# Performance work log

Hardware: AMD Instinct MI355X
Metric: run time of the kernel (lower is better)

The kernel has to match this reference:

```python
import jax, jax.numpy as jnp
import numpy as np

D_K = 128  # query/key dim, used for the 1/sqrt(d_k) scale


def setup_inputs() -> dict:
    key = jax.random.key(0)
    k1, k2, k3, k4 = jax.random.split(key, 4)
    B, L, d_model, d_k, d_v = 4, 2048, 1024, 128, 128

    def xavier(k, shape):
        # matches nn.init.xavier_uniform_ for 2D weights
        limit = np.sqrt(6.0 / (shape[0] + shape[1]))
        return jax.random.uniform(k, shape, jnp.float32, -limit, limit)

    return {
        "X": jax.random.normal(k1, (B, L, d_model), jnp.float32),
        "W_Q": xavier(k2, (d_model, d_k)),
        "W_K": xavier(k3, (d_model, d_k)),
        "W_V": xavier(k4, (d_model, d_v)),
    }


def reference(X, W_Q, W_K, W_V):
    # X: (B, L, d_model)
    L = X.shape[1]
    Q = jnp.einsum("bld,dk->blk", X, W_Q)          # (B, L, d_k)
    K = jnp.einsum("bld,dk->blk", X, W_K)          # (B, L, d_k)
    V = jnp.einsum("bld,dv->blv", X, W_V)          # (B, L, d_v)
    scale = D_K ** -0.5
    scores = jnp.einsum("bqk,bpk->bqp", Q, K) * scale  # (B, L, L)
    # causal mask: positions above the diagonal set to -inf
    causal = jnp.tril(jnp.ones((L, L), dtype=bool))
    scores = jnp.where(causal, scores, -jnp.inf)
    A = jax.nn.softmax(scores, axis=-1)            # (B, L, L)
    Z = jnp.einsum("bqp,bpv->bqv", A, V)           # (B, L, d_v)
    return Z
```

## Files before the change

### kernel.cpp

```cpp
#include <hip/hip_runtime.h>
#include <hip/hip_bf16.h>

typedef __bf16 bf16;
typedef __attribute__((ext_vector_type(4))) __bf16 bf16x4;
typedef __attribute__((ext_vector_type(8))) __bf16 bf16x8;
typedef __attribute__((ext_vector_type(4))) float f32x4;

#define D_MODEL 1024
#define DK 128
#define LSEQ 2048
#define NQT 128
#define NB 4
#define SCALE2 (0.08838834764831845f * 1.4426950408889634f)

__global__ __launch_bounds__(256) void xb_kernel(
    const float* __restrict__ X, bf16* __restrict__ Xb)
{
    size_t i = ((size_t)blockIdx.x * 256 + threadIdx.x) * 8;
    f32x4 a = *reinterpret_cast<const f32x4*>(&X[i]);
    f32x4 b = *reinterpret_cast<const f32x4*>(&X[i + 4]);
    bf16x8 h;
    h[0]=(bf16)a[0]; h[1]=(bf16)a[1]; h[2]=(bf16)a[2]; h[3]=(bf16)a[3];
    h[4]=(bf16)b[0]; h[5]=(bf16)b[1]; h[6]=(bf16)b[2]; h[7]=(bf16)b[3];
    *reinterpret_cast<bf16x8*>(&Xb[i]) = h;
}

__global__ __launch_bounds__(256) void wt_kernel(
    const float* __restrict__ Wq, const float* __restrict__ Wk,
    const float* __restrict__ Wv, bf16* __restrict__ Wt)
{
    __shared__ bf16 tile[64][72];
    const float* W = (blockIdx.z == 0) ? Wq : (blockIdx.z == 1) ? Wk : Wv;
    int k0 = blockIdx.x * 64;
    int n0 = blockIdx.y * 64;
    int t  = threadIdx.x;
    #pragma unroll
    for (int i = 0; i < 16; ++i) {
        int idx = t + i * 256;
        int r = idx >> 6, c = idx & 63;
        tile[c][r] = (bf16)W[(size_t)(k0 + r) * DK + n0 + c];
    }
    __syncthreads();
    bf16* out = Wt + (size_t)blockIdx.z * DK * D_MODEL;
    #pragma unroll
    for (int i = 0; i < 16; ++i) {
        int idx = t + i * 256;
        int rr = idx >> 6, cc = idx & 63;
        out[(size_t)(n0 + rr) * D_MODEL + k0 + cc] = tile[rr][cc];
    }
}

__global__ __launch_bounds__(256) void proj_kernel(
    const bf16* __restrict__ Xb, const bf16* __restrict__ Wt,
    bf16* __restrict__ Qs, bf16* __restrict__ Kb, bf16* __restrict__ Vt)
{
    __shared__ bf16 Xs[64][72];
    __shared__ bf16 Ws[128][72];
    int mt = blockIdx.x, mat = blockIdx.y;
    const bf16* W = Wt + (size_t)mat * DK * D_MODEL;
    int t = threadIdx.x;
    int wave = t >> 6, lane = t & 63;
    int lq = lane & 15, g = lane >> 4;
    int row0 = mt * 64;

    f32x4 acc[4][2];
    #pragma unroll
    for (int m = 0; m < 4; ++m)
        #pragma unroll
        for (int n = 0; n < 2; ++n) acc[m][n] = f32x4{0.f, 0.f, 0.f, 0.f};

    bf16x8 rx[2], rw[4];
    auto LOADR = [&](int k0) {
        #pragma unroll
        for (int i = 0; i < 2; ++i) {
            int u = t + i * 256, r = u >> 3, c = u & 7;
            rx[i] = *reinterpret_cast<const bf16x8*>(
                &Xb[(size_t)(row0 + r) * D_MODEL + k0 + c * 8]);
        }
        #pragma unroll
        for (int i = 0; i < 4; ++i) {
            int u = t + i * 256, r = u >> 3, c = u & 7;
            rw[i] = *reinterpret_cast<const bf16x8*>(
                &W[(size_t)r * D_MODEL + k0 + c * 8]);
        }
    };
    auto STORER = [&]() {
        #pragma unroll
        for (int i = 0; i < 2; ++i) {
            int u = t + i * 256, r = u >> 3, c = u & 7;
            *reinterpret_cast<bf16x8*>(&Xs[r][c * 8]) = rx[i];
        }
        #pragma unroll
        for (int i = 0; i < 4; ++i) {
            int u = t + i * 256, r = u >> 3, c = u & 7;
            *reinterpret_cast<bf16x8*>(&Ws[r][c * 8]) = rw[i];
        }
    };

    LOADR(0);
    for (int ks = 0; ks < 16; ++ks) {
        __syncthreads();
        STORER();
        if (ks + 1 < 16) LOADR((ks + 1) * 64);
        __syncthreads();
        #pragma unroll
        for (int kk = 0; kk < 2; ++kk) {
            bf16x8 a[4];
            #pragma unroll
            for (int mr = 0; mr < 4; ++mr)
                a[mr] = *reinterpret_cast<const bf16x8*>(&Xs[mr * 16 + lq][kk * 32 + g * 8]);
            #pragma unroll
            for (int n = 0; n < 2; ++n) {
                bf16x8 bfr = *reinterpret_cast<const bf16x8*>(
                    &Ws[wave * 32 + n * 16 + lq][kk * 32 + g * 8]);
                #pragma unroll
                for (int mr = 0; mr < 4; ++mr)
                    acc[mr][n] = __builtin_amdgcn_mfma_f32_16x16x32_bf16(a[mr], bfr, acc[mr][n], 0, 0, 0);
            }
        }
    }
    #pragma unroll
    for (int mr = 0; mr < 4; ++mr) {
        int orow = row0 + mr * 16 + g * 4;
        #pragma unroll
        for (int n = 0; n < 2; ++n) {
            int col = wave * 32 + n * 16 + lq;
            if (mat == 0) {
                #pragma unroll
                for (int r = 0; r < 4; ++r)
                    Qs[(size_t)(orow + r) * DK + col] = (bf16)(acc[mr][n][r] * SCALE2);
            } else if (mat == 1) {
                #pragma unroll
                for (int r = 0; r < 4; ++r)
                    Kb[(size_t)(orow + r) * DK + col] = (bf16)acc[mr][n][r];
            } else {
                int bb  = orow >> 11;
                int kv0 = orow & 2047;
                bf16x4 h;
                h[0]=(bf16)acc[mr][n][0]; h[1]=(bf16)acc[mr][n][1];
                h[2]=(bf16)acc[mr][n][2]; h[3]=(bf16)acc[mr][n][3];
                *reinterpret_cast<bf16x4*>(
                    &Vt[((size_t)bb * DK + col) * LSEQ + kv0]) = h;
            }
        }
    }
}

__global__ __launch_bounds__(256, 2) void attn_kernel(
    const bf16* __restrict__ Qs, const bf16* __restrict__ Kb,
    const bf16* __restrict__ Vt, float* __restrict__ Zp,
    float* __restrict__ Mp, float* __restrict__ Lp,
    float* __restrict__ Out, int S, int direct)
{
    __shared__ bf16 Ks[64][136];
    __shared__ bf16 Vs[128][72];
    __shared__ bf16 P[4][16][72];
    int bid = blockIdx.x;
    int b, qblk, s;
    if (S == 4) {
        int xcd = bid & 7, n = bid >> 3;
        b = xcd >> 1;
        int half = n >> 5, qraw = n & 31;
        qblk = half ? (31 - qraw) : qraw;
        s = ((xcd & 1) << 1) | half;
    } else {
        b = bid / (S * 32);
        int rem = bid % (S * 32);
        qblk = rem & 31;
        s = rem >> 5;
    }
    int t = threadIdx.x;
    int wave = t >> 6, lane = t & 63;
    int lq = lane & 15, g = lane >> 4;
    int qw16 = qblk * 4 + wave;
    int qg = qw16 * 16 + lq;

    int nt  = qblk + 1;
    int cpt = (nt + S - 1) / S;
    int t0  = s * cpt;
    int t1  = min(t0 + cpt, nt);

    const bf16* Kbase = Kb + (size_t)b * LSEQ * DK;
    const bf16* Vbase = Vt + (size_t)b * DK * LSEQ;

    const bf16* Qrow = Qs + ((size_t)b * LSEQ + qg) * DK;
    bf16x8 qf[4];
    #pragma unroll
    for (int ks = 0; ks < 4; ++ks)
        qf[ks] = *reinterpret_cast<const bf16x8*>(&Qrow[ks * 32 + g * 8]);

    f32x4 z[8];
    #pragma unroll
    for (int i = 0; i < 8; ++i) z[i] = f32x4{0.f, 0.f, 0.f, 0.f};
    float mrun = -3.0e38f, lrun = 0.f;

    bf16x8 kreg[4], vreg[4];
    auto LOADKV = [&](int kvb) {
        #pragma unroll
        for (int i = 0; i < 4; ++i) {
            int u = t + i * 256, r = u >> 4, c = u & 15;
            kreg[i] = *reinterpret_cast<const bf16x8*>(
                &Kbase[(size_t)(kvb + r) * DK + c * 8]);
        }
        #pragma unroll
        for (int i = 0; i < 4; ++i) {
            int u = t + i * 256, d = u >> 3, c = u & 7;
            vreg[i] = *reinterpret_cast<const bf16x8*>(
                &Vbase[(size_t)d * LSEQ + kvb + c * 8]);
        }
    };
    auto STOREKV = [&]() {
        #pragma unroll
        for (int i = 0; i < 4; ++i) {
            int u = t + i * 256, r = u >> 4, c = u & 15;
            *reinterpret_cast<bf16x8*>(&Ks[r][c * 8]) = kreg[i];
        }
        #pragma unroll
        for (int i = 0; i < 4; ++i) {
            int u = t + i * 256, d = u >> 3, c = u & 7;
            *reinterpret_cast<bf16x8*>(&Vs[d][c * 8]) = vreg[i];
        }
    };

    if (t0 < t1) {
        LOADKV(t0 * 64);
        for (int ti = t0; ti < t1; ++ti) {
            int kvb = ti * 64;
            __syncthreads();
            STOREKV();
            if (ti + 1 < t1) LOADKV((ti + 1) * 64);
            __syncthreads();

            f32x4 sc[4];
            #pragma unroll
            for (int jj = 0; jj < 4; ++jj) sc[jj] = f32x4{0.f, 0.f, 0.f, 0.f};
            #pragma unroll
            for (int jj = 0; jj < 4; ++jj)
                #pragma unroll
                for (int ks = 0; ks < 4; ++ks) {
                    bf16x8 a = *reinterpret_cast<const bf16x8*>(
                        &Ks[jj * 16 + lq][ks * 32 + g * 8]);
                    sc[jj] = __builtin_amdgcn_mfma_f32_16x16x32_bf16(a, qf[ks], sc[jj], 0, 0, 0);
                }

            float sv[16];
            if (ti == nt - 1) {
                #pragma unroll
                for (int jj = 0; jj < 4; ++jj)
                    #pragma unroll
                    for (int r = 0; r < 4; ++r) {
                        int kv0 = kvb + jj * 16 + g * 4 + r;
                        sv[jj * 4 + r] = (kv0 <= qg) ? sc[jj][r] : -3.0e38f;
                    }
            } else {
                #pragma unroll
                for (int jj = 0; jj < 4; ++jj)
                    #pragma unroll
                    for (int r = 0; r < 4; ++r) sv[jj * 4 + r] = sc[jj][r];
            }
            float mt = sv[0];
            #pragma unroll
            for (int i = 1; i < 16; ++i) mt = fmaxf(mt, sv[i]);
            mt = fmaxf(mt, __shfl_xor(mt, 16));
            mt = fmaxf(mt, __shfl_xor(mt, 32));
            if (!__all(mt <= mrun)) {
                float mnew  = fmaxf(mrun, mt);
                float alpha = exp2f(mrun - mnew);
                lrun *= alpha;
                #pragma unroll
                for (int i = 0; i < 8; ++i) {
                    z[i][0] *= alpha; z[i][1] *= alpha; z[i][2] *= alpha; z[i][3] *= alpha;
                }
                mrun = mnew;
            }
            float psum = 0.f;
            #pragma unroll
            for (int jj = 0; jj < 4; ++jj) {
                bf16x4 pb;
                #pragma unroll
                for (int r = 0; r < 4; ++r) {
                    float e = exp2f(sv[jj * 4 + r] - mrun);
                    psum += e;
                    pb[r] = (bf16)e;
                }
                *reinterpret_cast<bf16x4*>(&P[wave][lq][jj * 16 + g * 4]) = pb;
            }
            psum += __shfl_xor(psum, 16);
            psum += __shfl_xor(psum, 32);
            lrun += psum;
            #pragma unroll
            for (int sl = 0; sl < 2; ++sl) {
                bf16x8 pf = *reinterpret_cast<const bf16x8*>(&P[wave][lq][sl * 32 + g * 8]);
                #pragma unroll
                for (int dt = 0; dt < 8; ++dt) {
                    bf16x8 av = *reinterpret_cast<const bf16x8*>(
                        &Vs[dt * 16 + lq][sl * 32 + g * 8]);
                    z[dt] = __builtin_amdgcn_mfma_f32_16x16x32_bf16(av, pf, z[dt], 0, 0, 0);
                }
            }
        }
    }

    if (direct) {
        float inv = 1.f / lrun;
        float* orow = Out + ((size_t)b * LSEQ + qg) * DK;
        #pragma unroll
        for (int dt = 0; dt < 8; ++dt) {
            f32x4 v;
            v[0]=z[dt][0]*inv; v[1]=z[dt][1]*inv; v[2]=z[dt][2]*inv; v[3]=z[dt][3]*inv;
            *reinterpret_cast<f32x4*>(&orow[dt * 16 + g * 4]) = v;
        }
    } else {
        size_t T = ((size_t)(b * NQT + qw16) * S + s);
        float* zp = Zp + T * (16 * 128);
        #pragma unroll
        for (int dt = 0; dt < 8; ++dt)
            *reinterpret_cast<f32x4*>(&zp[lq * 128 + dt * 16 + g * 4]) = z[dt];
        if (g == 0) {
            Mp[T * 16 + lq] = mrun;
            Lp[T * 16 + lq] = lrun;
        }
    }
}

__global__ __launch_bounds__(256) void combine_kernel(
    const float* __restrict__ Zp, const float* __restrict__ Mp,
    const float* __restrict__ Lp, float* __restrict__ Out, int S)
{
    int qt = blockIdx.x, b = blockIdx.y;
    int t  = threadIdx.x;
    int r  = t >> 4;
    int d0 = (t & 15) * 8;
    size_t Tbase = (size_t)(b * NQT + qt) * S;

    float m = -3.0e38f;
    for (int s = 0; s < S; ++s)
        m = fmaxf(m, Mp[(Tbase + s) * 16 + r]);

    float L = 0.f;
    f32x4 a0 = {0.f,0.f,0.f,0.f}, a1 = {0.f,0.f,0.f,0.f};
    for (int s = 0; s < S; ++s) {
        float w = exp2f(Mp[(Tbase + s) * 16 + r] - m);
        L += w * Lp[(Tbase + s) * 16 + r];
        const float* zp = Zp + (Tbase + s) * (16 * 128) + r * 128 + d0;
        f32x4 v0 = *reinterpret_cast<const f32x4*>(&zp[0]);
        f32x4 v1 = *reinterpret_cast<const f32x4*>(&zp[4]);
        a0[0]+=w*v0[0]; a0[1]+=w*v0[1]; a0[2]+=w*v0[2]; a0[3]+=w*v0[3];
        a1[0]+=w*v1[0]; a1[1]+=w*v1[1]; a1[2]+=w*v1[2]; a1[3]+=w*v1[3];
    }
    float inv = 1.f / L;
    float* orow = Out + ((size_t)b * LSEQ + qt * 16 + r) * DK + d0;
    f32x4 o0, o1;
    o0[0]=a0[0]*inv; o0[1]=a0[1]*inv; o0[2]=a0[2]*inv; o0[3]=a0[3]*inv;
    o1[0]=a1[0]*inv; o1[1]=a1[1]*inv; o1[2]=a1[2]*inv; o1[3]=a1[3]*inv;
    *reinterpret_cast<f32x4*>(&orow[0]) = o0;
    *reinterpret_cast<f32x4*>(&orow[4]) = o1;
}

extern "C" void kernel_launch(void* const* d_in, const int* in_sizes, int n_in,
                              void* d_out, int out_size, void* d_ws, size_t ws_size,
                              hipStream_t stream)
{
    const float* X  = (const float*)d_in[0];
    const float* Wq = (const float*)d_in[1];
    const float* Wk = (const float*)d_in[2];
    const float* Wv = (const float*)d_in[3];
    float* Out = (float*)d_out;

    char* ws = (char*)d_ws;
    bf16* Wt = (bf16*)(ws);
    bf16* Xb = (bf16*)(ws + ((size_t)1 << 20));
    bf16* Qs = (bf16*)(ws + ((size_t)17 << 20));
    bf16* Kb = (bf16*)(ws + ((size_t)19 << 20));
    bf16* Vt = (bf16*)(ws + ((size_t)21 << 20));
    size_t base = (size_t)23 << 20;

    auto need = [](int S) -> size_t {
        return ((size_t)23 << 20) + (size_t)S * ((size_t)NB * NQT * 16 * 128 * 4)
                                  + (size_t)S * 2 * ((size_t)NB * NQT * 16 * 4);
    };
    int S = 1;
    if      (ws_size >= need(4)) S = 4;
    else if (ws_size >= need(2)) S = 2;

    float* Zp = (float*)(ws + base);
    float* Mp = (float*)(ws + base + (size_t)S * NB * NQT * 16 * 128 * 4);
    float* Lp = (float*)(ws + base + (size_t)S * NB * NQT * 16 * 128 * 4
                                   + (size_t)S * NB * NQT * 16 * 4);

    hipLaunchKernelGGL(wt_kernel,   dim3(16, 2, 3), dim3(256), 0, stream, Wq, Wk, Wv, Wt);
    hipLaunchKernelGGL(xb_kernel,   dim3(4096),     dim3(256), 0, stream, X, Xb);
    hipLaunchKernelGGL(proj_kernel, dim3(128, 3),   dim3(256), 0, stream, Xb, Wt, Qs, Kb, Vt);
    hipLaunchKernelGGL(attn_kernel, dim3(S * 32 * NB), dim3(256), 0, stream,
                       Qs, Kb, Vt, Zp, Mp, Lp, Out, S, (S == 1) ? 1 : 0);
    if (S > 1)
        hipLaunchKernelGGL(combine_kernel, dim3(NQT, NB), dim3(256), 0, stream,
                           Zp, Mp, Lp, Out, S);
}
```

Measured before the change: 58.81 us.

## Fuse X bf16 conversion into projection, raise attention occupancy, add MFMA priority hints

Removes the separate X-to-bf16 conversion kernel and has the projection kernel load fp32 X directly and convert while staging into shared memory. This drops one launch plus a full write and re-read of the bf16 copy of X. Separately, the attention kernel's launch bounds go from 2 to 3 blocks per CU, and s_setprio is raised around the MFMA loops. The fused projection now reads fp32 X three times (once per Q/K/V matrix), doubling its X load traffic, and the tighter register budget may cause spills in attention.

```diff
diff --git a/kernel.cpp b/kernel.cpp
--- a/kernel.cpp
+++ b/kernel.cpp
@@ -13,18 +13,6 @@
 #define NB 4
 #define SCALE2 (0.08838834764831845f * 1.4426950408889634f)
 
-__global__ __launch_bounds__(256) void xb_kernel(
-    const float* __restrict__ X, bf16* __restrict__ Xb)
-{
-    size_t i = ((size_t)blockIdx.x * 256 + threadIdx.x) * 8;
-    f32x4 a = *reinterpret_cast<const f32x4*>(&X[i]);
-    f32x4 b = *reinterpret_cast<const f32x4*>(&X[i + 4]);
-    bf16x8 h;
-    h[0]=(bf16)a[0]; h[1]=(bf16)a[1]; h[2]=(bf16)a[2]; h[3]=(bf16)a[3];
-    h[4]=(bf16)b[0]; h[5]=(bf16)b[1]; h[6]=(bf16)b[2]; h[7]=(bf16)b[3];
-    *reinterpret_cast<bf16x8*>(&Xb[i]) = h;
-}
-
 __global__ __launch_bounds__(256) void wt_kernel(
     const float* __restrict__ Wq, const float* __restrict__ Wk,
     const float* __restrict__ Wv, bf16* __restrict__ Wt)
@@ -51,7 +39,7 @@
 }
 
 __global__ __launch_bounds__(256) void proj_kernel(
-    const bf16* __restrict__ Xb, const bf16* __restrict__ Wt,
+    const float* __restrict__ X, const bf16* __restrict__ Wt,
     bf16* __restrict__ Qs, bf16* __restrict__ Kb, bf16* __restrict__ Vt)
 {
     __shared__ bf16 Xs[64][72];
@@ -69,31 +57,35 @@
         #pragma unroll
         for (int n = 0; n < 2; ++n) acc[m][n] = f32x4{0.f, 0.f, 0.f, 0.f};
 
-    bf16x8 rx[2], rw[4];
+    f32x4  rxf[4];
+    bf16x8 rw[4];
     auto LOADR = [&](int k0) {
         #pragma unroll
-        for (int i = 0; i < 2; ++i) {
-            int u = t + i * 256, r = u >> 3, c = u & 7;
-            rx[i] = *reinterpret_cast<const bf16x8*>(
-                &Xb[(size_t)(row0 + r) * D_MODEL + k0 + c * 8]);
-        }
-        #pragma unroll
-        for (int i = 0; i < 4; ++i) {
-            int u = t + i * 256, r = u >> 3, c = u & 7;
+        for (int i = 0; i < 4; ++i) {
+            int u = t + i * 256, r = u >> 4, c4 = u & 15;
+            rxf[i] = *reinterpret_cast<const f32x4*>(
+                &X[(size_t)(row0 + r) * D_MODEL + k0 + c4 * 4]);
+        }
+        #pragma unroll
+        for (int i = 0; i < 4; ++i) {
+            int u = t + i * 256, r = u >> 3, c8 = u & 7;
             rw[i] = *reinterpret_cast<const bf16x8*>(
-                &W[(size_t)r * D_MODEL + k0 + c * 8]);
+                &W[(size_t)r * D_MODEL + k0 + c8 * 8]);
         }
     };
     auto STORER = [&]() {
         #pragma unroll
-        for (int i = 0; i < 2; ++i) {
-            int u = t + i * 256, r = u >> 3, c = u & 7;
-            *reinterpret_cast<bf16x8*>(&Xs[r][c * 8]) = rx[i];
-        }
-        #pragma unroll
-        for (int i = 0; i < 4; ++i) {
-            int u = t + i * 256, r = u >> 3, c = u & 7;
-            *reinterpret_cast<bf16x8*>(&Ws[r][c * 8]) = rw[i];
+        for (int i = 0; i < 4; ++i) {
+            int u = t + i * 256, r = u >> 4, c4 = u & 15;
+            bf16x4 h;
+            h[0]=(bf16)rxf[i][0]; h[1]=(bf16)rxf[i][1];
+            h[2]=(bf16)rxf[i][2]; h[3]=(bf16)rxf[i][3];
+            *reinterpret_cast<bf16x4*>(&Xs[r][c4 * 4]) = h;
+        }
+        #pragma unroll
+        for (int i = 0; i < 4; ++i) {
+            int u = t + i * 256, r = u >> 3, c8 = u & 7;
+            *reinterpret_cast<bf16x8*>(&Ws[r][c8 * 8]) = rw[i];
         }
     };
 
@@ -146,7 +138,7 @@
     }
 }
 
-__global__ __launch_bounds__(256, 2) void attn_kernel(
+__global__ __launch_bounds__(256, 3) void attn_kernel(
     const bf16* __restrict__ Qs, const bf16* __restrict__ Kb,
     const bf16* __restrict__ Vt, float* __restrict__ Zp,
     float* __restrict__ Mp, float* __restrict__ Lp,
@@ -234,6 +226,7 @@
             f32x4 sc[4];
             #pragma unroll
             for (int jj = 0; jj < 4; ++jj) sc[jj] = f32x4{0.f, 0.f, 0.f, 0.f};
+            __builtin_amdgcn_s_setprio(1);
             #pragma unroll
             for (int jj = 0; jj < 4; ++jj)
                 #pragma unroll
@@ -242,6 +235,7 @@
                         &Ks[jj * 16 + lq][ks * 32 + g * 8]);
                     sc[jj] = __builtin_amdgcn_mfma_f32_16x16x32_bf16(a, qf[ks], sc[jj], 0, 0, 0);
                 }
+            __builtin_amdgcn_s_setprio(0);
 
             float sv[16];
             if (ti == nt - 1) {
@@ -288,6 +282,7 @@
             psum += __shfl_xor(psum, 16);
             psum += __shfl_xor(psum, 32);
             lrun += psum;
+            __builtin_amdgcn_s_setprio(1);
             #pragma unroll
             for (int sl = 0; sl < 2; ++sl) {
                 bf16x8 pf = *reinterpret_cast<const bf16x8*>(&P[wave][lq][sl * 32 + g * 8]);
@@ -298,6 +293,7 @@
                     z[dt] = __builtin_amdgcn_mfma_f32_16x16x32_bf16(av, pf, z[dt], 0, 0, 0);
                 }
             }
+            __builtin_amdgcn_s_setprio(0);
         }
     }
 
@@ -369,15 +365,14 @@
 
     char* ws = (char*)d_ws;
     bf16* Wt = (bf16*)(ws);
-    bf16* Xb = (bf16*)(ws + ((size_t)1 << 20));
-    bf16* Qs = (bf16*)(ws + ((size_t)17 << 20));
-    bf16* Kb = (bf16*)(ws + ((size_t)19 << 20));
-    bf16* Vt = (bf16*)(ws + ((size_t)21 << 20));
-    size_t base = (size_t)23 << 20;
+    bf16* Qs = (bf16*)(ws + ((size_t)1 << 20));
+    bf16* Kb = (bf16*)(ws + ((size_t)3 << 20));
+    bf16* Vt = (bf16*)(ws + ((size_t)5 << 20));
+    size_t base = (size_t)7 << 20;
 
     auto need = [](int S) -> size_t {
-        return ((size_t)23 << 20) + (size_t)S * ((size_t)NB * NQT * 16 * 128 * 4)
-                                  + (size_t)S * 2 * ((size_t)NB * NQT * 16 * 4);
+        return ((size_t)7 << 20) + (size_t)S * ((size_t)NB * NQT * 16 * 128 * 4)
+                                 + (size_t)S * 2 * ((size_t)NB * NQT * 16 * 4);
     };
     int S = 1;
     if      (ws_size >= need(4)) S = 4;
@@ -389,8 +384,7 @@
                                    + (size_t)S * NB * NQT * 16 * 4);
 
     hipLaunchKernelGGL(wt_kernel,   dim3(16, 2, 3), dim3(256), 0, stream, Wq, Wk, Wv, Wt);
-    hipLaunchKernelGGL(xb_kernel,   dim3(4096),     dim3(256), 0, stream, X, Xb);
-    hipLaunchKernelGGL(proj_kernel, dim3(128, 3),   dim3(256), 0, stream, Xb, Wt, Qs, Kb, Vt);
+    hipLaunchKernelGGL(proj_kernel, dim3(128, 3),   dim3(256), 0, stream, X, Wt, Qs, Kb, Vt);
     hipLaunchKernelGGL(attn_kernel, dim3(S * 32 * NB), dim3(256), 0, stream,
                        Qs, Kb, Vt, Zp, Mp, Lp, Out, S, (S == 1) ? 1 : 0);
     if (S > 1)
```

Measured after the change: 51.77 us. 1.14x faster.
